# Kernel tuning notes

Measured on AMD Instinct MI355X. Metric: run time of the kernel, lower is better.

The kernel has to match this reference:

```python
import jax, jax.numpy as jnp
import numpy as np

N_NODES = 50000
N_EDGES = 800000
IN_DIM = 16
H1, H2, H3, HFC = 64, 128, 256, 256


def setup_inputs() -> dict:
    key = jax.random.key(0)
    ks = jax.random.split(key, 8)
    w = lambda k, s: jax.random.normal(k, s, dtype=jnp.float32) * 0.05
    return {
        "X": jax.random.normal(ks[0], (N_NODES, IN_DIM), dtype=jnp.float32),
        "edge_index": jax.random.randint(ks[1], (2, N_EDGES), 0, N_NODES, dtype=jnp.int64),
        "W1": w(ks[2], (2 * IN_DIM, H1)), "b1": jnp.zeros((H1,), jnp.float32),
        "W2": w(ks[3], (2 * H1, H2)), "b2": jnp.zeros((H2,), jnp.float32),
        "W3": w(ks[4], (2 * H2, H3)), "b3": jnp.zeros((H3,), jnp.float32),
        "Wf1": w(ks[5], (H3, HFC)), "bf1": jnp.zeros((HFC,), jnp.float32),
        "Wf2": w(ks[6], (HFC, 1)), "bf2": jnp.zeros((1,), jnp.float32),
    }


def edge_conv(x, edge_index, W, b):
    # EdgeConv (DGCNN): msg = ReLU(Linear([x_i, x_j - x_i])), max-aggregate at i
    src, dst = edge_index[0], edge_index[1]
    xi = x[dst]                      # [E, d] target node feats
    xj = x[src]                      # [E, d] source node feats
    msg = jax.nn.relu(jnp.concatenate([xi, xj - xi], axis=-1) @ W + b)  # [E, out]
    agg = jax.ops.segment_max(msg, dst, num_segments=x.shape[0])        # [N, out]
    # nodes with no incoming edge get -inf from segment_max -> zero them
    return jnp.where(jnp.isneginf(agg), 0.0, agg)


def reference(X, edge_index, W1, b1, W2, b2, W3, b3, Wf1, bf1, Wf2, bf2):
    H = edge_conv(X, edge_index, W1, b1)
    H = edge_conv(H, edge_index, W2, b2)
    H = edge_conv(H, edge_index, W3, b3)
    # MLP head (dropout is identity at inference)
    H = jax.nn.relu(H @ Wf1 + bf1)
    out = jax.nn.sigmoid(H @ Wf2 + bf2)
    return out.squeeze(-1)  # [N]
```

## Files before the change

### kernel.cpp

```cpp
#include <hip/hip_runtime.h>
#include <math.h>

#define NN 50000
#define NE 800000

typedef unsigned short ushort_t;
typedef __attribute__((ext_vector_type(8))) short bf16x8;
typedef __attribute__((ext_vector_type(4))) float f32x4;

__device__ inline unsigned short f2bf(float f) {
    unsigned int u = __float_as_uint(f);
    u = (u + 0x7fffu + ((u >> 16) & 1u)) >> 16;
    return (unsigned short)u;
}
__device__ inline unsigned int pack2bf(float lo, float hi) {
    return (unsigned int)f2bf(lo) | ((unsigned int)f2bf(hi) << 16);
}

__global__ void prep0_kernel(const int* __restrict__ ei, int istride,
                             int* __restrict__ esrc32, int* __restrict__ edst32,
                             int* __restrict__ deg) {
    int i = blockIdx.x * blockDim.x + threadIdx.x;
    int s = gridDim.x * blockDim.x;
    for (int j = i; j < NN; j += s) deg[j] = 0;
    const int* eis = ei;
    const int* eid = ei + (size_t)NE * istride;
    for (int j = i; j < NE; j += s) {
        esrc32[j] = eis[(size_t)j * istride];
        edst32[j] = eid[(size_t)j * istride];
    }
}

__global__ void hist_kernel(const int* __restrict__ edst, int* __restrict__ deg, int nE) {
    int i = blockIdx.x * blockDim.x + threadIdx.x;
    int s = gridDim.x * blockDim.x;
    for (; i < nE; i += s) atomicAdd(&deg[edst[i]], 1);
}

__global__ __launch_bounds__(256)
void scan_reduce(const int* __restrict__ deg, int* __restrict__ bsum, int n) {
    __shared__ int s[256];
    const int t = threadIdx.x;
    const int i = blockIdx.x * 256 + t;
    s[t] = (i < n) ? deg[i] : 0;
    __syncthreads();
#pragma unroll
    for (int off = 128; off > 0; off >>= 1) {
        if (t < off) s[t] += s[t + off];
        __syncthreads();
    }
    if (t == 0) bsum[blockIdx.x] = s[0];
}

__global__ __launch_bounds__(256)
void scan_tops(const int* __restrict__ bsum, int* __restrict__ boff,
               int* __restrict__ rowptr, int nb, int n) {
    __shared__ int s[256];
    const int t = threadIdx.x;
    const int v = (t < nb) ? bsum[t] : 0;
    s[t] = v;
    __syncthreads();
    for (int off = 1; off < 256; off <<= 1) {
        int u = (t >= off) ? s[t - off] : 0;
        __syncthreads();
        s[t] += u;
        __syncthreads();
    }
    if (t < nb) boff[t] = s[t] - v;
    if (t == 255) rowptr[n] = s[255];
}

__global__ __launch_bounds__(256)
void scan_apply(int* __restrict__ deg, const int* __restrict__ boff,
                int* __restrict__ rowptr, int n) {
    __shared__ int s[256];
    const int t = threadIdx.x;
    const int i = blockIdx.x * 256 + t;
    const int v = (i < n) ? deg[i] : 0;
    s[t] = v;
    __syncthreads();
    for (int off = 1; off < 256; off <<= 1) {
        int u = (t >= off) ? s[t - off] : 0;
        __syncthreads();
        s[t] += u;
        __syncthreads();
    }
    if (i < n) {
        int ex = boff[blockIdx.x] + s[t] - v;
        rowptr[i] = ex;
        deg[i] = ex;
    }
}

__global__ void scatter_kernel(const int* __restrict__ esrc, const int* __restrict__ edst,
                               int* __restrict__ cursor, int* __restrict__ col, int nE) {
    int i = blockIdx.x * blockDim.x + threadIdx.x;
    int s = gridDim.x * blockDim.x;
    for (; i < nE; i += s) {
        int d = edst[i];
        int pos = atomicAdd(&cursor[d], 1);
        col[pos] = esrc[i];
    }
}

__global__ void megaprep_kernel(const float* __restrict__ W1, const float* __restrict__ W2,
                                const float* __restrict__ W3, const float* __restrict__ Wf1,
                                const float* __restrict__ X,
                                ushort_t* __restrict__ Wt1, ushort_t* __restrict__ Wt2,
                                ushort_t* __restrict__ Wt3, ushort_t* __restrict__ Wf1t,
                                ushort_t* __restrict__ Xb, float* __restrict__ hacc) {
    const int T0 = 128 * 32;
    const int T1 = T0 + 256 * 64;
    const int T2 = T1 + 512 * 128;
    const int T3 = T2 + 256 * 256;
    const int T4 = T3 + NN * 32;
    const int T5 = T4 + NN;
    int i = blockIdx.x * blockDim.x + threadIdx.x;
    int s = gridDim.x * blockDim.x;
    for (; i < T5; i += s) {
        if (i < T0) {
            int idx = i, o = idx / 32, k = idx % 32;
            float v = 0.f;
            if (k < 16)
                v = (o < 64) ? (W1[k * 64 + o] - W1[(k + 16) * 64 + o])
                             : W1[(k + 16) * 64 + (o - 64)];
            Wt1[idx] = f2bf(v);
        } else if (i < T1) {
            int idx = i - T0, o = idx / 64, k = idx % 64;
            float v = (o < 128) ? (W2[k * 128 + o] - W2[(k + 64) * 128 + o])
                                : W2[(k + 64) * 128 + (o - 128)];
            Wt2[idx] = f2bf(v);
        } else if (i < T2) {
            int idx = i - T1, o = idx / 128, k = idx % 128;
            float v = (o < 256) ? (W3[(size_t)k * 256 + o] - W3[(size_t)(k + 128) * 256 + o])
                                : W3[(size_t)(k + 128) * 256 + (o - 256)];
            Wt3[idx] = f2bf(v);
        } else if (i < T3) {
            int idx = i - T2, nn = idx / 256, k = idx % 256;
            Wf1t[idx] = f2bf(Wf1[(size_t)k * 256 + nn]);
        } else if (i < T4) {
            int idx = i - T3, row = idx >> 5, c = idx & 31;
            Xb[idx] = (c < 16) ? f2bf(X[(size_t)row * 16 + c]) : (ushort_t)0;
        } else {
            hacc[i - T4] = 0.f;
        }
    }
}

template<int K, int OUT, int NF, int MR>
__global__ __launch_bounds__(256, 3)
void gemm_mfma(const ushort_t* __restrict__ A, const ushort_t* __restrict__ Wt,
               const float* __restrict__ bias, ushort_t* __restrict__ PQ, int n) {
    constexpr int NOUT = 2 * OUT;
    constexpr int KB = K / 32;
    __shared__ ushort_t lds[128][132];

    const int wave = threadIdx.x >> 6;
    const int lane = threadIdx.x & 63;
    const int lr = lane & 15;
    const int kg = lane >> 4;
    const int row0b = blockIdx.x * (4 * MR * 16);
    const int row0 = row0b + wave * (MR * 16);
    const int col0 = blockIdx.y * (NF * 16);

    f32x4 acc[MR][NF];
#pragma unroll
    for (int m = 0; m < MR; ++m)
#pragma unroll
        for (int f = 0; f < NF; ++f) acc[m][f] = (f32x4)(0.f);

    const ushort_t* Ap[MR];
#pragma unroll
    for (int m = 0; m < MR; ++m) {
        int arow = row0 + m * 16 + lr;
        if (arow >= n) arow = n - 1;
        Ap[m] = A + (size_t)arow * K + kg * 8;
    }
    const ushort_t* Bp = Wt + (size_t)(col0 + lr) * K + kg * 8;

    bf16x8 af[2][MR];
    bf16x8 bfv[2][NF];
#pragma unroll
    for (int m = 0; m < MR; ++m) af[0][m] = *(const bf16x8*)(Ap[m]);
#pragma unroll
    for (int f = 0; f < NF; ++f) bfv[0][f] = *(const bf16x8*)(Bp + (size_t)f * 16 * K);

#pragma unroll
    for (int kb = 0; kb < KB; ++kb) {
        const int cur = kb & 1, nxt = cur ^ 1;
        if (kb + 1 < KB) {
#pragma unroll
            for (int m = 0; m < MR; ++m)
                af[nxt][m] = *(const bf16x8*)(Ap[m] + (kb + 1) * 32);
#pragma unroll
            for (int f = 0; f < NF; ++f)
                bfv[nxt][f] = *(const bf16x8*)(Bp + (size_t)f * 16 * K + (kb + 1) * 32);
        }
#pragma unroll
        for (int f = 0; f < NF; ++f)
#pragma unroll
            for (int m = 0; m < MR; ++m)
                acc[m][f] = __builtin_amdgcn_mfma_f32_16x16x32_bf16(af[cur][m], bfv[cur][f], acc[m][f], 0, 0, 0);
    }

#pragma unroll
    for (int m = 0; m < MR; ++m) {
#pragma unroll
        for (int f = 0; f < NF; ++f) {
            int cg = col0 + f * 16 + lr;
            float bb = (cg < OUT) ? bias[cg] : 0.f;
#pragma unroll
            for (int r = 0; r < 4; ++r) {
                lds[wave * (MR * 16) + m * 16 + kg * 4 + r][f * 16 + lr] =
                    f2bf(acc[m][f][r] + bb);
            }
        }
    }
    __syncthreads();

    const int t = threadIdx.x;
#pragma unroll
    for (int it = 0; it < 8; ++it) {
        int j = it * 256 + t;
        int row = j >> 4;
        int q = j & 15;
        int grow = row0b + row;
        if (grow < n) {
            uint4 v = *(const uint4*)(&lds[row][q * 8]);
            *(uint4*)(PQ + (size_t)grow * NOUT + col0 + q * 8) = v;
        }
    }
}

__global__ __launch_bounds__(256, 4)
void head_mfma(const ushort_t* __restrict__ H, const ushort_t* __restrict__ Wf1t,
               const float* __restrict__ bf1, const float* __restrict__ Wf2,
               float* __restrict__ hacc, int n) {
    const int wave = threadIdx.x >> 6;
    const int lane = threadIdx.x & 63;
    const int row0 = (blockIdx.x * 4 + wave) * 16;
    const int col0 = blockIdx.y * 128;
    const int lr = lane & 15;
    const int kg = lane >> 4;

    f32x4 acc[8];
#pragma unroll
    for (int i = 0; i < 8; ++i) acc[i] = (f32x4)(0.f);

    int arow = row0 + lr;
    if (arow >= n) arow = n - 1;
    const ushort_t* Aptr = H + (size_t)arow * 256 + kg * 8;
    const ushort_t* Bp = Wf1t + (size_t)(col0 + lr) * 256 + kg * 8;

    bf16x8 afb[2], bfb[2][8];
    afb[0] = *(const bf16x8*)(Aptr);
#pragma unroll
    for (int nf = 0; nf < 8; ++nf) bfb[0][nf] = *(const bf16x8*)(Bp + (size_t)nf * 16 * 256);

#pragma unroll
    for (int kb = 0; kb < 8; ++kb) {
        const int cur = kb & 1, nxt = cur ^ 1;
        if (kb + 1 < 8) {
            afb[nxt] = *(const bf16x8*)(Aptr + (kb + 1) * 32);
#pragma unroll
            for (int nf = 0; nf < 8; ++nf)
                bfb[nxt][nf] = *(const bf16x8*)(Bp + (size_t)nf * 16 * 256 + (kb + 1) * 32);
        }
#pragma unroll
        for (int nf = 0; nf < 8; ++nf)
            acc[nf] = __builtin_amdgcn_mfma_f32_16x16x32_bf16(afb[cur], bfb[cur][nf], acc[nf], 0, 0, 0);
    }

    float part[4] = {0.f, 0.f, 0.f, 0.f};
#pragma unroll
    for (int nf = 0; nf < 8; ++nf) {
        int c = col0 + nf * 16 + lr;
        float w2 = Wf2[c];
        float bb = bf1[c];
#pragma unroll
        for (int r = 0; r < 4; ++r)
            part[r] = fmaf(fmaxf(acc[nf][r] + bb, 0.f), w2, part[r]);
    }
#pragma unroll
    for (int s = 1; s < 16; s <<= 1) {
#pragma unroll
        for (int r = 0; r < 4; ++r) part[r] += __shfl_xor(part[r], s, 16);
    }
    if (lr == 0) {
#pragma unroll
        for (int r = 0; r < 4; ++r) {
            int row = row0 + kg * 4 + r;
            if (row < n) atomicAdd(&hacc[row], part[r]);
        }
    }
}

__global__ void sigmoid_kernel(const float* __restrict__ hacc, const float* __restrict__ bf2,
                               float* __restrict__ out, int n) {
    int i = blockIdx.x * blockDim.x + threadIdx.x;
    int s = gridDim.x * blockDim.x;
    float b = bf2[0];
    for (; i < n; i += s) out[i] = 1.f / (1.f + expf(-(hacc[i] + b)));
}

template<int OUT>
__global__ __launch_bounds__(256, 8)
void segmax_combine(const ushort_t* __restrict__ PQ, const int* __restrict__ rowptr,
                    const int* __restrict__ col, ushort_t* __restrict__ Hout, int n) {
    constexpr int NOUT = 2 * OUT;
    constexpr int G = OUT / 8;
    constexpr int NPB = 256 / G;
    const int gid = threadIdx.x / G;
    const int lane = threadIdx.x % G;
    const int i = blockIdx.x * NPB + gid;
    if (i >= n) return;

    const int r0 = rowptr[i];
    const int r1 = rowptr[i + 1];
    const int c8 = lane * 8;

    float m[8];
#pragma unroll
    for (int j = 0; j < 8; ++j) m[j] = -INFINITY;

    auto domax = [&](uint4 q) {
        m[0] = fmaxf(m[0], __uint_as_float(q.x << 16));
        m[1] = fmaxf(m[1], __uint_as_float(q.x & 0xffff0000u));
        m[2] = fmaxf(m[2], __uint_as_float(q.y << 16));
        m[3] = fmaxf(m[3], __uint_as_float(q.y & 0xffff0000u));
        m[4] = fmaxf(m[4], __uint_as_float(q.z << 16));
        m[5] = fmaxf(m[5], __uint_as_float(q.z & 0xffff0000u));
        m[6] = fmaxf(m[6], __uint_as_float(q.w << 16));
        m[7] = fmaxf(m[7], __uint_as_float(q.w & 0xffff0000u));
    };

    int r = r0;
    for (; r + 3 < r1; r += 4) {
        int s0 = col[r], s1 = col[r + 1], s2 = col[r + 2], s3 = col[r + 3];
        uint4 q0 = *(const uint4*)(PQ + (size_t)s0 * NOUT + OUT + c8);
        uint4 q1 = *(const uint4*)(PQ + (size_t)s1 * NOUT + OUT + c8);
        uint4 q2 = *(const uint4*)(PQ + (size_t)s2 * NOUT + OUT + c8);
        uint4 q3 = *(const uint4*)(PQ + (size_t)s3 * NOUT + OUT + c8);
        domax(q0); domax(q1); domax(q2); domax(q3);
    }
    for (; r < r1; ++r) {
        domax(*(const uint4*)(PQ + (size_t)col[r] * NOUT + OUT + c8));
    }

    const uint4 pb = *(const uint4*)(PQ + (size_t)i * NOUT + c8);
    float p[8];
    p[0] = __uint_as_float(pb.x << 16); p[1] = __uint_as_float(pb.x & 0xffff0000u);
    p[2] = __uint_as_float(pb.y << 16); p[3] = __uint_as_float(pb.y & 0xffff0000u);
    p[4] = __uint_as_float(pb.z << 16); p[5] = __uint_as_float(pb.z & 0xffff0000u);
    p[6] = __uint_as_float(pb.w << 16); p[7] = __uint_as_float(pb.w & 0xffff0000u);

    float h[8];
#pragma unroll
    for (int j = 0; j < 8; ++j) h[j] = fmaxf(p[j] + m[j], 0.f);

    uint4 o;
    o.x = pack2bf(h[0], h[1]);
    o.y = pack2bf(h[2], h[3]);
    o.z = pack2bf(h[4], h[5]);
    o.w = pack2bf(h[6], h[7]);
    *(uint4*)(Hout + (size_t)i * OUT + c8) = o;
}

extern "C" void kernel_launch(void* const* d_in, const int* in_sizes, int n_in,
                              void* d_out, int out_size, void* d_ws, size_t ws_size,
                              hipStream_t stream) {
    const float* X   = (const float*)d_in[0];
    const int*   ei  = (const int*)d_in[1];
    const float* W1  = (const float*)d_in[2];
    const float* b1  = (const float*)d_in[3];
    const float* W2  = (const float*)d_in[4];
    const float* b2  = (const float*)d_in[5];
    const float* W3  = (const float*)d_in[6];
    const float* b3  = (const float*)d_in[7];
    const float* Wf1 = (const float*)d_in[8];
    const float* bf1 = (const float*)d_in[9];
    const float* Wf2 = (const float*)d_in[10];
    const float* bf2 = (const float*)d_in[11];
    float* out = (float*)d_out;

    int istride = (in_sizes[1] == 4 * NE) ? 2 : 1;

    ushort_t* PQ     = (ushort_t*)d_ws;
    ushort_t* Ha     = PQ + (size_t)NN * 512;
    ushort_t* Hb     = Ha + (size_t)NN * 256;
    int*      rowptr = (int*)(Hb + (size_t)NN * 256);
    int*      deg    = rowptr + (NN + 8);
    int*      col    = deg + NN;
    int*      esrc32 = col + NE;
    int*      edst32 = esrc32 + NE;
    int*      bsum   = edst32 + NE;
    int*      boff   = bsum + 256;
    ushort_t* Wt1    = (ushort_t*)(boff + 256);
    ushort_t* Wt2    = Wt1 + 128 * 32;
    ushort_t* Wt3    = Wt2 + 256 * 64;
    ushort_t* Wf1t   = Wt3 + 512 * 128;
    ushort_t* Xb     = Wf1t + 256 * 256;
    float*    hacc   = (float*)(Xb + (size_t)NN * 32);

    const int NB = (NN + 255) / 256;

    prep0_kernel<<<1024, 256, 0, stream>>>(ei, istride, esrc32, edst32, deg);
    hist_kernel<<<1024, 256, 0, stream>>>(edst32, deg, NE);
    scan_reduce<<<NB, 256, 0, stream>>>(deg, bsum, NN);
    scan_tops<<<1, 256, 0, stream>>>(bsum, boff, rowptr, NB, NN);
    scan_apply<<<NB, 256, 0, stream>>>(deg, boff, rowptr, NN);
    scatter_kernel<<<1024, 256, 0, stream>>>(esrc32, edst32, deg, col, NE);

    megaprep_kernel<<<1024, 256, 0, stream>>>(W1, W2, W3, Wf1, X,
                                              Wt1, Wt2, Wt3, Wf1t, Xb, hacc);

    const int GB = (NN + 127) / 128;

    {
        dim3 g(GB, 1);
        gemm_mfma<32, 64, 8, 2><<<g, 256, 0, stream>>>(Xb, Wt1, b1, PQ, NN);
    }
    segmax_combine<64><<<(NN + 31) / 32, 256, 0, stream>>>(PQ, rowptr, col, Ha, NN);

    {
        dim3 g(GB, 2);
        gemm_mfma<64, 128, 8, 2><<<g, 256, 0, stream>>>(Ha, Wt2, b2, PQ, NN);
    }
    segmax_combine<128><<<(NN + 15) / 16, 256, 0, stream>>>(PQ, rowptr, col, Hb, NN);

    {
        dim3 g(GB, 4);
        gemm_mfma<128, 256, 8, 2><<<g, 256, 0, stream>>>(Hb, Wt3, b3, PQ, NN);
    }
    segmax_combine<256><<<(NN + 7) / 8, 256, 0, stream>>>(PQ, rowptr, col, Ha, NN);

    {
        dim3 g((NN + 63) / 64, 2);
        head_mfma<<<g, 256, 0, stream>>>(Ha, Wf1t, bf1, Wf2, hacc, NN);
    }
    sigmoid_kernel<<<64, 256, 0, stream>>>(hacc, bf2, out, NN);
}
```

Baseline: 349.0 us.

## Retile head GEMM with LDS-staged weights and 64x64 per-wave tiles

The MLP head kernel now stages a 64-column slice of Wf1 in padded shared memory once per block. Each wave computes a 64-row by 64-column tile (4x4 MFMA fragments) instead of a 16x128 strip. Before, every wave reloaded its full B strip from global memory, so this cuts B traffic and gives more reuse of A and B per MFMA. In exchange it uses more registers and about 33KB of LDS per block, and the launch-bounds occupancy hint drops from 4 to 3.

```diff
diff --git a/kernel.cpp b/kernel.cpp
--- a/kernel.cpp
+++ b/kernel.cpp
@@ -232,66 +232,94 @@
     }
 }
 
-__global__ __launch_bounds__(256, 4)
+__global__ __launch_bounds__(256, 3)
 void head_mfma(const ushort_t* __restrict__ H, const ushort_t* __restrict__ Wf1t,
                const float* __restrict__ bf1, const float* __restrict__ Wf2,
                float* __restrict__ hacc, int n) {
-    const int wave = threadIdx.x >> 6;
-    const int lane = threadIdx.x & 63;
-    const int row0 = (blockIdx.x * 4 + wave) * 16;
-    const int col0 = blockIdx.y * 128;
+    __shared__ ushort_t ldsB[64 * 264];
+
+    const int t = threadIdx.x;
+    const int wave = t >> 6;
+    const int lane = t & 63;
     const int lr = lane & 15;
     const int kg = lane >> 4;
-
-    f32x4 acc[8];
-#pragma unroll
-    for (int i = 0; i < 8; ++i) acc[i] = (f32x4)(0.f);
-
-    int arow = row0 + lr;
-    if (arow >= n) arow = n - 1;
-    const ushort_t* Aptr = H + (size_t)arow * 256 + kg * 8;
-    const ushort_t* Bp = Wf1t + (size_t)(col0 + lr) * 256 + kg * 8;
-
-    bf16x8 afb[2], bfb[2][8];
-    afb[0] = *(const bf16x8*)(Aptr);
-#pragma unroll
-    for (int nf = 0; nf < 8; ++nf) bfb[0][nf] = *(const bf16x8*)(Bp + (size_t)nf * 16 * 256);
+    const int row0 = blockIdx.x * 256 + wave * 64;
+    const int col0 = blockIdx.y * 64;
+
+#pragma unroll
+    for (int it = 0; it < 8; ++it) {
+        int j = it * 256 + t;
+        int row = j >> 5;
+        int q = j & 31;
+        uint4 v = *(const uint4*)(Wf1t + (size_t)(col0 + row) * 256 + q * 8);
+        *(uint4*)(&ldsB[row * 264 + q * 8]) = v;
+    }
+    __syncthreads();
+
+    f32x4 acc[4][4];
+#pragma unroll
+    for (int m = 0; m < 4; ++m)
+#pragma unroll
+        for (int f = 0; f < 4; ++f) acc[m][f] = (f32x4)(0.f);
+
+    const ushort_t* Ap[4];
+#pragma unroll
+    for (int m = 0; m < 4; ++m) {
+        int arow = row0 + m * 16 + lr;
+        if (arow >= n) arow = n - 1;
+        Ap[m] = H + (size_t)arow * 256 + kg * 8;
+    }
+    const ushort_t* Bl = ldsB + lr * 264 + kg * 8;
 
 #pragma unroll
     for (int kb = 0; kb < 8; ++kb) {
-        const int cur = kb & 1, nxt = cur ^ 1;
-        if (kb + 1 < 8) {
-            afb[nxt] = *(const bf16x8*)(Aptr + (kb + 1) * 32);
-#pragma unroll
-            for (int nf = 0; nf < 8; ++nf)
-                bfb[nxt][nf] = *(const bf16x8*)(Bp + (size_t)nf * 16 * 256 + (kb + 1) * 32);
-        }
-#pragma unroll
-        for (int nf = 0; nf < 8; ++nf)
-            acc[nf] = __builtin_amdgcn_mfma_f32_16x16x32_bf16(afb[cur], bfb[cur][nf], acc[nf], 0, 0, 0);
-    }
-
-    float part[4] = {0.f, 0.f, 0.f, 0.f};
-#pragma unroll
-    for (int nf = 0; nf < 8; ++nf) {
-        int c = col0 + nf * 16 + lr;
+        bf16x8 af[4];
+#pragma unroll
+        for (int m = 0; m < 4; ++m) af[m] = *(const bf16x8*)(Ap[m] + kb * 32);
+        bf16x8 bfv[4];
+#pragma unroll
+        for (int f = 0; f < 4; ++f)
+            bfv[f] = *(const bf16x8*)(Bl + f * 16 * 264 + kb * 32);
+#pragma unroll
+        for (int f = 0; f < 4; ++f)
+#pragma unroll
+            for (int m = 0; m < 4; ++m)
+                acc[m][f] = __builtin_amdgcn_mfma_f32_16x16x32_bf16(af[m], bfv[f], acc[m][f], 0, 0, 0);
+    }
+
+    float part[4][4];
+#pragma unroll
+    for (int m = 0; m < 4; ++m)
+#pragma unroll
+        for (int r = 0; r < 4; ++r) part[m][r] = 0.f;
+
+#pragma unroll
+    for (int f = 0; f < 4; ++f) {
+        int c = col0 + f * 16 + lr;
         float w2 = Wf2[c];
         float bb = bf1[c];
 #pragma unroll
-        for (int r = 0; r < 4; ++r)
-            part[r] = fmaf(fmaxf(acc[nf][r] + bb, 0.f), w2, part[r]);
+        for (int m = 0; m < 4; ++m)
+#pragma unroll
+            for (int r = 0; r < 4; ++r)
+                part[m][r] = fmaf(fmaxf(acc[m][f][r] + bb, 0.f), w2, part[m][r]);
     }
 #pragma unroll
     for (int s = 1; s < 16; s <<= 1) {
 #pragma unroll
-        for (int r = 0; r < 4; ++r) part[r] += __shfl_xor(part[r], s, 16);
+        for (int m = 0; m < 4; ++m)
+#pragma unroll
+            for (int r = 0; r < 4; ++r)
+                part[m][r] += __shfl_xor(part[m][r], s, 16);
     }
     if (lr == 0) {
 #pragma unroll
-        for (int r = 0; r < 4; ++r) {
-            int row = row0 + kg * 4 + r;
-            if (row < n) atomicAdd(&hacc[row], part[r]);
-        }
+        for (int m = 0; m < 4; ++m)
+#pragma unroll
+            for (int r = 0; r < 4; ++r) {
+                int row = row0 + m * 16 + kg * 4 + r;
+                if (row < n) atomicAdd(&hacc[row], part[m][r]);
+            }
     }
 }
 
@@ -435,7 +463,7 @@
     segmax_combine<256><<<(NN + 7) / 8, 256, 0, stream>>>(PQ, rowptr, col, Ha, NN);
 
     {
-        dim3 g((NN + 63) / 64, 2);
+        dim3 g((NN + 255) / 256, 4);
         head_mfma<<<g, 256, 0, stream>>>(Ha, Wf1t, bf1, Wf2, hacc, NN);
     }
     sigmoid_kernel<<<64, 256, 0, stream>>>(hacc, bf2, out, NN);
```

Result: faster. 310.2 us, median of 2 (-11.1%).
